# Optimization experiments

Measured on AMD Instinct MI355X. Metric: run time of the kernel, lower is better.

## Reference

```python
import jax, jax.numpy as jnp
import numpy as np

H = 2048
W = 2048
N = H * W
NUM_CC = 1 << 20
N_ITERS = 20  # pointer-doubling covers tree depth up to 2**20 (actual depth ~ e*ln N ~ 45)
EPS = 1e-10


def _log_scaling(f):
    # f: [NUM_CC, 15] = xmin, ymin, xmax, ymax, area, angle, pca_big, pca_small, hu1..hu7
    # -> [NUM_CC, 17] = xmin..ymax, log(area), signed-log(pca_big, pca_small, hu1..hu7), lshape, cos(angle), sin(angle)
    lshape = jnp.sqrt(f[:, 7:8]) / (jnp.sqrt(f[:, 6:7]) + EPS)
    cosangle = jnp.cos(f[:, 5:6])
    sinangle = jnp.sin(f[:, 5:6])
    log_area = jnp.log(f[:, 4:5])
    signed_log = jnp.log(jnp.abs(f[:, 6:]) + EPS) * jnp.sign(f[:, 6:])
    return jnp.concatenate([f[:, :4], log_area, signed_log, lshape, cosangle, sinangle], axis=1)


def _tree_path_sum(contrib, parent):
    # out[p] = sum of contrib over p and all its ancestors (root has parent == -1).
    # Parallel pointer-doubling: after k steps acc[i] sums contrib over 2**k chain nodes.
    acc, par = contrib, parent
    for _ in range(N_ITERS):
        valid = par >= 0
        pidx = jnp.where(valid, par, 0)
        acc = acc + jnp.where(valid, acc[pidx], jnp.zeros((), acc.dtype))
        par = jnp.where(valid, par[pidx], -1)
    return acc


def setup_inputs() -> dict:
    rng = np.random.default_rng(0)
    # random recursive tree: parent[i] uniform in [0, i), root = node 0
    parent = (rng.random(N) * np.arange(N)).astype(np.int32)
    parent[0] = -1
    cc_id = rng.integers(0, NUM_CC, size=N).astype(np.int32)
    diff = rng.standard_normal(N).astype(np.float32)
    attrs = np.empty((NUM_CC, 15), np.float32)
    attrs[:, :4] = rng.random((NUM_CC, 4)) * 100.0          # bbox coords
    attrs[:, 4] = rng.random(NUM_CC) * 1000.0 + 1.0         # area (>0 for log)
    attrs[:, 5] = rng.standard_normal(NUM_CC)               # angle
    attrs[:, 6:8] = rng.random((NUM_CC, 2)) + 0.01          # pca_big/pca_small (>=0 for sqrt)
    attrs[:, 8:] = rng.standard_normal((NUM_CC, 7)).astype(np.float32)  # hu moments
    weight = ((rng.random((17, 1)) - 0.5) * 0.02).astype(np.float32)
    bias = np.zeros((1,), np.float32)
    return {
        "diff": jnp.asarray(diff),
        "attributes": jnp.asarray(attrs),
        "weight": jnp.asarray(weight),
        "bias": jnp.asarray(bias),
        "parent": jnp.asarray(parent),
        "cc_id": jnp.asarray(cc_id),
    }


def reference(diff, attributes, weight, bias, parent, cc_id):
    rescaled = _log_scaling(attributes)                                   # [NUM_CC, 17]
    cc_scores = jax.nn.sigmoid(rescaled @ weight + bias[None, :])[:, 0]   # [NUM_CC]
    contrib = diff * cc_scores[cc_id]                                     # [N]
    out = _tree_path_sum(contrib, parent)                                 # [N]
    return out.reshape(H, W)
```

## Files before the change

kernel.cpp:

```cpp
#include <hip/hip_runtime.h>

#define EPSF 1e-10f

struct alignas(8) Node { int par; float c; };

typedef int   v4i __attribute__((ext_vector_type(4)));
typedef float v4f __attribute__((ext_vector_type(4)));

__device__ __forceinline__ float signed_log(float x) {
    float sg = (x > 0.f) ? 1.f : ((x < 0.f) ? -1.f : 0.f);
    return logf(fabsf(x) + EPSF) * sg;
}

__global__ void scores_kernel(const float* __restrict__ attrs,
                              const float* __restrict__ weight,
                              const float* __restrict__ bias,
                              float* __restrict__ scores, int num_cc) {
    int i = blockIdx.x * blockDim.x + threadIdx.x;
    if (i >= num_cc) return;
    const float* f = attrs + (long long)i * 15;
    float w[17];
#pragma unroll
    for (int k = 0; k < 17; ++k) w[k] = weight[k];
    float acc = bias[0];
    acc += w[0] * f[0] + w[1] * f[1] + w[2] * f[2] + w[3] * f[3];
    acc += w[4] * logf(f[4]);
#pragma unroll
    for (int j = 0; j < 9; ++j) acc += w[5 + j] * signed_log(f[6 + j]);
    float lshape = sqrtf(f[7]) / (sqrtf(f[6]) + EPSF);
    acc += w[14] * lshape;
    acc += w[15] * cosf(f[5]);
    acc += w[16] * sinf(f[5]);
    __builtin_nontemporal_store(1.f / (1.f + expf(-acc)), &scores[i]);
}

__global__ void pack_kernel4(const v4f* __restrict__ diff4,
                             const v4i* __restrict__ parent4,
                             const v4i* __restrict__ cc4,
                             const float* __restrict__ scores,
                             v4i* __restrict__ packed2, int n4) {
    int i = blockIdx.x * blockDim.x + threadIdx.x;
    if (i >= n4) return;
    v4f d = __builtin_nontemporal_load(&diff4[i]);
    v4i p = __builtin_nontemporal_load(&parent4[i]);
    v4i c = __builtin_nontemporal_load(&cc4[i]);
    float s0 = scores[c.x], s1 = scores[c.y], s2 = scores[c.z], s3 = scores[c.w];
    v4i o0, o1;
    o0.x = p.x; o0.y = __float_as_int(d.x * s0);
    o0.z = p.y; o0.w = __float_as_int(d.y * s1);
    o1.x = p.z; o1.y = __float_as_int(d.z * s2);
    o1.z = p.w; o1.w = __float_as_int(d.w * s3);
    __builtin_nontemporal_store(o0, &packed2[2 * i]);
    __builtin_nontemporal_store(o1, &packed2[2 * i + 1]);
}

__global__ void pack_kernel(const float* __restrict__ diff,
                            const int* __restrict__ parent,
                            const int* __restrict__ cc_id,
                            const float* __restrict__ scores,
                            Node* __restrict__ packed, int lo, int n) {
    int i = lo + blockIdx.x * blockDim.x + threadIdx.x;
    if (i >= n) return;
    Node nd;
    nd.par = parent[i];
    nd.c = diff[i] * scores[cc_id[i]];
    packed[i] = nd;
}

__device__ __forceinline__ void load_self_nt(const Node* p, int i, int& par, float& c) {
    long long raw = __builtin_nontemporal_load((const long long*)(p + i));
    par = (int)(raw & 0xffffffffLL);
    c = __int_as_float((int)(raw >> 32));
}

__global__ void walk_base(const Node* __restrict__ packed,
                          float* __restrict__ out, int range_end) {
    int i = blockIdx.x * blockDim.x + threadIdx.x;
    if (i >= range_end) return;
    int cur; float s;
    load_self_nt(packed, i, cur, s);
    while (cur >= 0) {
        Node nd = packed[cur];
        s += nd.c;
        cur = nd.par;
    }
    __builtin_nontemporal_store(s, &out[i]);
}

__global__ void walk_phase(const Node* __restrict__ packed,
                           float* __restrict__ out, int lo, int hi) {
    int i = lo + blockIdx.x * blockDim.x + threadIdx.x;
    if (i >= hi) return;
    int cur; float s;
    load_self_nt(packed, i, cur, s);
    while (cur >= lo) {
        Node nd = packed[cur];
        s += nd.c;
        cur = nd.par;
    }
    s += out[cur];
    __builtin_nontemporal_store(s, &out[i]);
}

__global__ void walk_base2(const int* __restrict__ parent,
                           const float* __restrict__ contrib,
                           float* __restrict__ out, int range_end) {
    int i = blockIdx.x * blockDim.x + threadIdx.x;
    if (i >= range_end) return;
    float s = 0.f;
    int cur = i;
    while (cur >= 0) { s += contrib[cur]; cur = parent[cur]; }
    out[i] = s;
}

__global__ void walk_phase2(const int* __restrict__ parent,
                            const float* __restrict__ contrib,
                            float* __restrict__ out, int lo, int hi) {
    int i = lo + blockIdx.x * blockDim.x + threadIdx.x;
    if (i >= hi) return;
    float s = 0.f;
    int cur = i;
    while (cur >= lo) { s += contrib[cur]; cur = parent[cur]; }
    s += out[cur];
    out[i] = s;
}

__global__ void contrib_kernel(const float* __restrict__ diff,
                               const int* __restrict__ cc_id,
                               const float* __restrict__ scores,
                               float* __restrict__ contrib, int n) {
    int i = blockIdx.x * blockDim.x + threadIdx.x;
    if (i >= n) return;
    contrib[i] = diff[i] * scores[cc_id[i]];
}

static inline int iminh(int a, int b) { return a < b ? a : b; }

extern "C" void kernel_launch(void* const* d_in, const int* in_sizes, int n_in,
                              void* d_out, int out_size, void* d_ws, size_t ws_size,
                              hipStream_t stream) {
    const float* diff   = (const float*)d_in[0];
    const float* attrs  = (const float*)d_in[1];
    const float* weight = (const float*)d_in[2];
    const float* bias   = (const float*)d_in[3];
    const int*   parent = (const int*)d_in[4];
    const int*   cc_id  = (const int*)d_in[5];
    float* out = (float*)d_out;

    const int n      = in_sizes[0];
    const int num_cc = in_sizes[1] / 15;

    float* scores = (float*)d_ws;
    const size_t scores_bytes = (size_t)num_cc * sizeof(float);
    const size_t packed_need  = scores_bytes + (size_t)n * sizeof(Node);
    const bool use_packed = ws_size >= packed_need;

    const int TB = 256;
    scores_kernel<<<(num_cc + TB - 1) / TB, TB, 0, stream>>>(attrs, weight, bias, scores, num_cc);

    const int BASE   = 131072;
    const int R2_MIN = 1 << 19;

    if (use_packed) {
        Node* packed = (Node*)((char*)d_ws + scores_bytes);
        if ((n & 3) == 0) {
            pack_kernel4<<<(n / 4 + TB - 1) / TB, TB, 0, stream>>>(
                (const v4f*)diff, (const v4i*)parent, (const v4i*)cc_id, scores, (v4i*)packed, n / 4);
        } else {
            pack_kernel<<<(n + TB - 1) / TB, TB, 0, stream>>>(diff, parent, cc_id, scores, packed, 0, n);
        }
        int base_end = iminh(BASE, n);
        walk_base<<<(base_end + TB - 1) / TB, TB, 0, stream>>>(packed, out, base_end);
        int lo = base_end;
        while (lo < n) {
            int ratio = (lo < R2_MIN) ? 4 : 2;
            long long hi_ll = (long long)lo * ratio;
            int hi = (hi_ll > n) ? n : (int)hi_ll;
            walk_phase<<<((hi - lo) + TB - 1) / TB, TB, 0, stream>>>(packed, out, lo, hi);
            lo = hi;
        }
    } else {
        float* contrib = (float*)((char*)d_ws + scores_bytes);
        contrib_kernel<<<(n + TB - 1) / TB, TB, 0, stream>>>(diff, cc_id, scores, contrib, n);
        int base_end = iminh(BASE, n);
        walk_base2<<<(base_end + TB - 1) / TB, TB, 0, stream>>>(parent, contrib, out, base_end);
        int lo = base_end;
        while (lo < n) {
            int ratio = (lo < R2_MIN) ? 4 : 2;
            long long hi_ll = (long long)lo * ratio;
            int hi = (hi_ll > n) ? n : (int)hi_ll;
            walk_phase2<<<((hi - lo) + TB - 1) / TB, TB, 0, stream>>>(parent, contrib, out, lo, hi);
            lo = hi;
        }
    }
}
```

Baseline: 130.5 us.

## Walk multiple nodes per thread in phase kernels for memory-level parallelism

Replaces the one-node-per-thread phase walk with a templated kernel where each thread walks 4 or 8 consecutive nodes at once, interleaving their pointer-chasing loads. The self loads and the output stores become vectorized 16-byte accesses. The goal is to hide the latency of dependent gathers by keeping several independent chains in flight per thread. In exchange, threads stay busy until their longest chain finishes and use more registers, which can cost occupancy.

```diff
diff --git a/kernel.cpp b/kernel.cpp
--- a/kernel.cpp
+++ b/kernel.cpp
@@ -67,18 +67,14 @@
     packed[i] = nd;
 }
 
-__device__ __forceinline__ void load_self_nt(const Node* p, int i, int& par, float& c) {
-    long long raw = __builtin_nontemporal_load((const long long*)(p + i));
-    par = (int)(raw & 0xffffffffLL);
-    c = __int_as_float((int)(raw >> 32));
-}
 
 __global__ void walk_base(const Node* __restrict__ packed,
                           float* __restrict__ out, int range_end) {
     int i = blockIdx.x * blockDim.x + threadIdx.x;
     if (i >= range_end) return;
-    int cur; float s;
-    load_self_nt(packed, i, cur, s);
+    long long raw = __builtin_nontemporal_load((const long long*)(packed + i));
+    int cur = (int)(raw & 0xffffffffLL);
+    float s = __int_as_float((int)(raw >> 32));
     while (cur >= 0) {
         Node nd = packed[cur];
         s += nd.c;
@@ -87,19 +83,58 @@
     __builtin_nontemporal_store(s, &out[i]);
 }
 
-__global__ void walk_phase(const Node* __restrict__ packed,
-                           float* __restrict__ out, int lo, int hi) {
-    int i = lo + blockIdx.x * blockDim.x + threadIdx.x;
-    if (i >= hi) return;
-    int cur; float s;
-    load_self_nt(packed, i, cur, s);
-    while (cur >= lo) {
-        Node nd = packed[cur];
-        s += nd.c;
-        cur = nd.par;
-    }
-    s += out[cur];
-    __builtin_nontemporal_store(s, &out[i]);
+template <int PX>
+__global__ void walk_phaseN(const Node* __restrict__ packed,
+                            float* __restrict__ out, int lo, int hi) {
+    long long t = (long long)blockIdx.x * blockDim.x + threadIdx.x;
+    int base = lo + (int)(t * PX);
+    if (base >= hi) return;
+    int cur[PX]; float s[PX];
+
+    if (base + PX <= hi) {
+#pragma unroll
+        for (int k = 0; k < PX; k += 2) {
+            v4i raw = __builtin_nontemporal_load((const v4i*)(packed + base + k));
+            cur[k]     = raw.x; s[k]     = __int_as_float(raw.y);
+            cur[k + 1] = raw.z; s[k + 1] = __int_as_float(raw.w);
+        }
+    } else {
+#pragma unroll
+        for (int k = 0; k < PX; ++k) {
+            if (base + k < hi) { Node nd = packed[base + k]; cur[k] = nd.par; s[k] = nd.c; }
+            else               { cur[k] = 0; s[k] = 0.f; }
+        }
+    }
+
+    while (true) {
+        bool any = false;
+#pragma unroll
+        for (int k = 0; k < PX; ++k) any |= (cur[k] >= lo);
+        if (!__any(any)) break;
+#pragma unroll
+        for (int k = 0; k < PX; ++k) {
+            bool act = cur[k] >= lo;
+            int idx = act ? cur[k] : lo;
+            Node nd = packed[idx];
+            s[k]  += act ? nd.c : 0.f;
+            cur[k] = act ? nd.par : cur[k];
+        }
+    }
+
+#pragma unroll
+    for (int k = 0; k < PX; ++k) s[k] += out[cur[k]];
+
+    if (base + PX <= hi) {
+#pragma unroll
+        for (int k = 0; k < PX; k += 4) {
+            v4f o; o.x = s[k]; o.y = s[k + 1]; o.z = s[k + 2]; o.w = s[k + 3];
+            __builtin_nontemporal_store(o, (v4f*)(out + base + k));
+        }
+    } else {
+#pragma unroll
+        for (int k = 0; k < PX; ++k)
+            if (base + k < hi) out[base + k] = s[k];
+    }
 }
 
 __global__ void walk_base2(const int* __restrict__ parent,
@@ -160,6 +195,7 @@
 
     const int BASE   = 131072;
     const int R2_MIN = 1 << 19;
+    const int PX8_MIN = 1 << 20;
 
     if (use_packed) {
         Node* packed = (Node*)((char*)d_ws + scores_bytes);
@@ -176,7 +212,14 @@
             int ratio = (lo < R2_MIN) ? 4 : 2;
             long long hi_ll = (long long)lo * ratio;
             int hi = (hi_ll > n) ? n : (int)hi_ll;
-            walk_phase<<<((hi - lo) + TB - 1) / TB, TB, 0, stream>>>(packed, out, lo, hi);
+            int cnt = hi - lo;
+            if (cnt >= PX8_MIN) {
+                long long threads = (cnt + 7) / 8;
+                walk_phaseN<8><<<(int)((threads + TB - 1) / TB), TB, 0, stream>>>(packed, out, lo, hi);
+            } else {
+                long long threads = (cnt + 3) / 4;
+                walk_phaseN<4><<<(int)((threads + TB - 1) / TB), TB, 0, stream>>>(packed, out, lo, hi);
+            }
             lo = hi;
         }
     } else {
```

Result: no change. 133.1 us (+2.0%).
